# Optimization experiments

Measured on AMD Instinct MI355X. Metric: run time of the kernel, lower is better.

## Reference

```python
import jax, jax.numpy as jnp
import numpy as np

NUM_HEADS = 4
NUM_GROUPS = 8
EPS = 1e-5


def group_norm(x, w, b):
    # x: (B, C, H, W); normalize per group of C//NUM_GROUPS channels
    B, C, H, W = x.shape
    xg = x.reshape(B, NUM_GROUPS, C // NUM_GROUPS, H, W)
    mean = xg.mean(axis=(2, 3, 4), keepdims=True)
    var = xg.var(axis=(2, 3, 4), keepdims=True)
    xn = ((xg - mean) * jax.lax.rsqrt(var + EPS)).reshape(B, C, H, W)
    return xn * w[None, :, None, None] + b[None, :, None, None]


def conv1x1(x, w, b):
    # x: (B, C_in, H, W), w: (C_out, C_in), b: (C_out,)
    return jnp.einsum('bchw,oc->bohw', x, w) + b[None, :, None, None]


def setup_inputs() -> dict:
    key = jax.random.key(0)
    B, C, H, W = 4, 256, 64, 64
    k1, k2, k3 = jax.random.split(key, 3)
    scale = 1.0 / np.sqrt(C)
    return {
        'x': jax.random.normal(k1, (B, C, H, W), dtype=jnp.float32),
        'norm_w': jnp.ones((C,), dtype=jnp.float32),
        'norm_b': jnp.zeros((C,), dtype=jnp.float32),
        'qkv_w': jax.random.normal(k2, (3 * C, C), dtype=jnp.float32) * scale,
        'qkv_b': jnp.zeros((3 * C,), dtype=jnp.float32),
        'proj_w': jax.random.normal(k3, (C, C), dtype=jnp.float32) * scale,
        'proj_b': jnp.zeros((C,), dtype=jnp.float32),
    }


def reference(x, norm_w, norm_b, qkv_w, qkv_b, proj_w, proj_b):
    B, C, H, W = x.shape
    hd = C // NUM_HEADS  # head dim
    h = group_norm(x, norm_w, norm_b)
    qkv = conv1x1(h, qkv_w, qkv_b)            # (B, 3C, H, W)
    q, k, v = jnp.split(qkv, 3, axis=1)
    q = q.reshape(B, NUM_HEADS, hd, H * W)
    k = k.reshape(B, NUM_HEADS, hd, H * W)
    v = v.reshape(B, NUM_HEADS, hd, H * W)
    attn = jnp.einsum('bhcn,bhcm->bhnm', q, k) / jnp.sqrt(jnp.asarray(hd, x.dtype))
    attn = jax.nn.softmax(attn, axis=-1)
    out = jnp.einsum('bhnm,bhcm->bhcn', attn, v).reshape(B, C, H, W)
    out = conv1x1(out, proj_w, proj_b)
    return x + out
```

## Files before the change

### kernel.cpp

```cpp
#include <hip/hip_runtime.h>
#include <hip/hip_bf16.h>
#include <stdint.h>


#define B_  4
#define C_  256
#define N_  4096
#define NH_ 4
#define HD_ 64
#define G_  8
#define CPG_ 32
#define GRP_ELEMS (CPG_ * N_)

typedef __attribute__((ext_vector_type(8))) short short8;
typedef __attribute__((ext_vector_type(4))) float f32x4;
typedef __attribute__((ext_vector_type(4))) unsigned short us4;

__device__ __forceinline__ unsigned short f2bf(float f) {
  union { float f; unsigned u; } v; v.f = f;
  unsigned r = v.u + 0x7FFFu + ((v.u >> 16) & 1u);
  return (unsigned short)(r >> 16);
}

__device__ __forceinline__ unsigned pkbf2(float a, float b) {
  __hip_bfloat162 h = __float22bfloat162_rn(make_float2(a, b));
  unsigned r; __builtin_memcpy(&r, &h, sizeof(r)); return r;
}

__device__ __forceinline__ void dma16(const unsigned short* g, unsigned short* l) {
  __builtin_amdgcn_global_load_lds(
      (const __attribute__((address_space(1))) unsigned int*)(g),
      (__attribute__((address_space(3))) unsigned int*)(l), 16, 0, 0);
}

__global__ void cvt_weights(const float* __restrict__ qkvw,
                            const float* __restrict__ projw,
                            unsigned short* __restrict__ wq,
                            unsigned short* __restrict__ wp) {
  int i = blockIdx.x * 256 + threadIdx.x;
  if (i < 768 * 256) wq[i] = f2bf(qkvw[i]);
  if (i < 256 * 256) wp[i] = f2bf(projw[i]);
}

__global__ void gn_partial(const float* __restrict__ x, float* __restrict__ partial) {
  int idx = blockIdx.x;
  int slice = idx & 15, g = (idx >> 4) & 7, b = idx >> 7;
  int t = threadIdx.x;
  const float* base = x + (size_t)(b * C_ + g * CPG_) * N_ + slice * 256;
  float s = 0.f, sq = 0.f;
#pragma unroll
  for (int cc = 0; cc < CPG_; cc++) {
    float v = base[(size_t)cc * N_ + t];
    s += v; sq += v * v;
  }
#pragma unroll
  for (int off = 32; off; off >>= 1) {
    s  += __shfl_down(s,  off, 64);
    sq += __shfl_down(sq, off, 64);
  }
  __shared__ float ls[8];
  int wave = t >> 6, lane = t & 63;
  if (lane == 0) { ls[wave * 2] = s; ls[wave * 2 + 1] = sq; }
  __syncthreads();
  if (t == 0) {
    float S = ls[0] + ls[2] + ls[4] + ls[6];
    float SQ = ls[1] + ls[3] + ls[5] + ls[7];
    partial[idx * 2] = S; partial[idx * 2 + 1] = SQ;
  }
}

__global__ void gn_finalize(const float* __restrict__ partial, float* __restrict__ stats) {
  int t = threadIdx.x;
  if (t < 32) {
    float s = 0.f, sq = 0.f;
    for (int i = 0; i < 16; i++) {
      s  += partial[(t * 16 + i) * 2];
      sq += partial[(t * 16 + i) * 2 + 1];
    }
    const float inv = 1.0f / (float)GRP_ELEMS;
    float mean = s * inv;
    float var = sq * inv - mean * mean;
    stats[t * 2] = mean;
    stats[t * 2 + 1] = rsqrtf(var + 1e-5f);
  }
}

__global__ void gn_apply(const float* __restrict__ x,
                         const float* __restrict__ nw, const float* __restrict__ nb,
                         const float* __restrict__ stats, unsigned short* __restrict__ hT) {
  int nt = blockIdx.x, ct = blockIdx.y, b = blockIdx.z;
  __shared__ unsigned short tile[32][72];
  int t = threadIdx.x;
  int n_loc = t & 63, c_loc = t >> 6;
  float mean = stats[(b * G_ + ct) * 2];
  float rstd = stats[(b * G_ + ct) * 2 + 1];
  const float* xb = x + (size_t)(b * C_ + ct * CPG_) * N_ + nt * 64;
#pragma unroll
  for (int rr = 0; rr < 8; rr++) {
    int cc = rr * 4 + c_loc;
    int c = ct * CPG_ + cc;
    float v = xb[(size_t)cc * N_ + n_loc];
    v = (v - mean) * rstd * nw[c] + nb[c];
    tile[cc][n_loc] = f2bf(v);
  }
  __syncthreads();
  int c2 = t & 31, n2 = t >> 5;
  unsigned short* out = hT + ((size_t)(b * N_ + nt * 64)) * C_ + ct * CPG_ + c2;
#pragma unroll
  for (int pass = 0; pass < 8; pass++) {
    int n = pass * 8 + n2;
    out[(size_t)n * C_] = tile[c2][n];
  }
}

__global__ __launch_bounds__(256) void qkv_gemm(
    const unsigned short* __restrict__ hT, const unsigned short* __restrict__ wq,
    const float* __restrict__ qb,
    unsigned short* __restrict__ Qt, unsigned short* __restrict__ Kt,
    unsigned short* __restrict__ V) {
  int nt = blockIdx.x, ot = blockIdx.y, b = blockIdx.z;
  int t = threadIdx.x;
  int wave = t >> 6, lane = t & 63, l15 = lane & 15, quad = lane >> 4, l7 = l15 & 7;
  int o_base = ot * 64 + wave * 16;

  __shared__ __align__(16) unsigned short sh[64 * C_];

  {
    int row0 = wave * 2 + (lane >> 5);
    int col8 = lane & 31;
    int src8 = (col8 & 24) | ((col8 & 7) ^ (row0 & 7));
    const unsigned short* gsrc = hT + ((size_t)(b * N_ + nt * 64 + row0)) * C_ + src8 * 8;
#pragma unroll
    for (int it = 0; it < 8; it++)
      dma16(gsrc + (size_t)it * 8 * C_, sh + (it * 8 + wave * 2) * C_);
  }

  f32x4 acc[4];
#pragma unroll
  for (int tt = 0; tt < 4; tt++) acc[tt] = (f32x4){0.f, 0.f, 0.f, 0.f};

  const short8* arow = reinterpret_cast<const short8*>(wq + (size_t)(o_base + l15) * C_);

  asm volatile("s_waitcnt vmcnt(0)" ::: "memory");
  __syncthreads();

#pragma unroll
  for (int kk = 0; kk < 8; kk++) {
    short8 a = arow[kk * 4 + quad];
    int g = kk * 4 + quad;
    int col8 = (g & 24) | ((g & 7) ^ l7);
#pragma unroll
    for (int tt = 0; tt < 4; tt++) {
      short8 bf = *reinterpret_cast<const short8*>(&sh[(tt * 16 + l15) * C_ + col8 * 8]);
      acc[tt] = __builtin_amdgcn_mfma_f32_16x16x32_bf16(a, bf, acc[tt], 0, 0, 0);
    }
  }

  int sec = ot >> 2, head = ot & 3;
  int cw = wave * 16 + quad * 4;
  int bh = b * NH_ + head;
  const float SC = 0.125f * 1.44269504088896340736f;

  if (sec == 0) {
#pragma unroll
    for (int tt = 0; tt < 4; tt++) {
      int n = nt * 64 + tt * 16 + l15;
      us4 pk;
#pragma unroll
      for (int i = 0; i < 4; i++)
        pk[i] = f2bf((acc[tt][i] + qb[ot * 64 + cw + i]) * SC);
      *reinterpret_cast<us4*>(Qt + ((size_t)bh * N_ + n) * HD_ + cw) = pk;
    }
  } else if (sec == 1) {
#pragma unroll
    for (int tt = 0; tt < 4; tt++) {
      int n = nt * 64 + tt * 16 + l15;
      us4 pk;
#pragma unroll
      for (int i = 0; i < 4; i++)
        pk[i] = f2bf(acc[tt][i] + qb[ot * 64 + cw + i]);
      *reinterpret_cast<us4*>(Kt + ((size_t)bh * N_ + n) * HD_ + cw) = pk;
    }
  } else {
#pragma unroll
    for (int tt = 0; tt < 4; tt++) {
      int n = nt * 64 + tt * 16 + l15;
#pragma unroll
      for (int i = 0; i < 4; i++)
        V[((size_t)bh * HD_ + cw + i) * N_ + n] = f2bf(acc[tt][i] + qb[ot * 64 + cw + i]);
    }
  }
}

__global__ __launch_bounds__(256, 2) void flash_attn(
    const unsigned short* __restrict__ Qt, const unsigned short* __restrict__ Kt,
    const unsigned short* __restrict__ Vv, unsigned short* __restrict__ aoT) {
  int bh = blockIdx.x & 15, qt = blockIdx.x >> 4;
  int b = bh >> 2, head = bh & 3;
  int t = threadIdx.x;
  int wave = t >> 6, lane = t & 63, l15 = lane & 15, quad = lane >> 4;
  int l7 = l15 & 7;
  int qsub = wave >> 1, khalf = wave & 1;

  const unsigned short* Qb = Qt + (size_t)bh * N_ * HD_;
  const unsigned short* Kb = Kt + (size_t)bh * N_ * HD_;
  const unsigned short* Vb = Vv + (size_t)bh * HD_ * N_;
  int q_base = qt * 128 + qsub * 64;

  __shared__ __align__(16) unsigned char smem[74752];
  unsigned short* Ks = (unsigned short*)smem;
  unsigned short* Vs = (unsigned short*)(smem + 32768);
  unsigned short* Ps = (unsigned short*)(smem + 65536);
  float* Obuf = (float*)smem;
  float* lbuf = (float*)(smem + 34816);

  const short8 vones = {(short)0x3F80, (short)0x3F80, (short)0x3F80, (short)0x3F80,
                        (short)0x3F80, (short)0x3F80, (short)0x3F80, (short)0x3F80};

  short8 qf[4][2];
#pragma unroll
  for (int r = 0; r < 4; r++)
#pragma unroll
    for (int h = 0; h < 2; h++)
      qf[r][h] = *reinterpret_cast<const short8*>(
          Qb + (size_t)(q_base + r * 16 + l15) * HD_ + h * 32 + quad * 8);

  f32x4 oa[4][4], la[4];
#pragma unroll
  for (int r = 0; r < 4; r++) {
    la[r] = (f32x4){0.f, 0.f, 0.f, 0.f};
#pragma unroll
    for (int ct = 0; ct < 4; ct++) oa[r][ct] = (f32x4){0.f, 0.f, 0.f, 0.f};
  }

  int i8 = lane >> 3, e = lane & 7;
  int perm = (e ^ i8) * 8;
  int kvoff = (khalf * 2) * 4096;
  auto stage = [&](int kt2, int buf) {
    int m0 = khalf * 2048 + kt2 * 64;
    unsigned short* Kd = Ks + kvoff + buf * 4096;
    unsigned short* Vd = Vs + kvoff + buf * 4096;
#pragma unroll
    for (int cc = 0; cc < 4; cc++) {
      int c = qsub * 4 + cc;
      dma16(Kb + (size_t)(m0 + c * 8 + i8) * HD_ + perm, Kd + c * 512);
      dma16(Vb + (size_t)(c * 8 + i8) * N_ + m0 + perm, Vd + c * 512);
    }
  };

  stage(0, 0);

  unsigned short* Pw = Ps + wave * 16 * 72;

#pragma unroll 1
  for (int kt = 0; kt < 32; kt++) {
    int buf = kt & 1;
    asm volatile("s_waitcnt vmcnt(0)" ::: "memory");
    __builtin_amdgcn_s_barrier();
    if (kt + 1 < 32) stage(kt + 1, buf ^ 1);

    const unsigned short* Kbuf = Ks + kvoff + buf * 4096;
    const unsigned short* Vbuf = Vs + kvoff + buf * 4096;

    short8 kf[4][2], vf[4][2];
#pragma unroll
    for (int tt = 0; tt < 4; tt++)
#pragma unroll
      for (int kh2 = 0; kh2 < 2; kh2++) {
        kf[tt][kh2] = *reinterpret_cast<const short8*>(
            &Kbuf[(tt * 16 + l15) * 64 + (((kh2 * 4 + quad) ^ l7) * 8)]);
        vf[tt][kh2] = *reinterpret_cast<const short8*>(
            &Vbuf[(tt * 16 + l15) * 64 + (((kh2 * 4 + quad) ^ l7) * 8)]);
      }

#pragma unroll
    for (int r = 0; r < 4; r++) {
      f32x4 s[4];
#pragma unroll
      for (int tt = 0; tt < 4; tt++) {
        f32x4 z = (f32x4){0.f, 0.f, 0.f, 0.f};
        z = __builtin_amdgcn_mfma_f32_16x16x32_bf16(kf[tt][0], qf[r][0], z, 0, 0, 0);
        s[tt] = __builtin_amdgcn_mfma_f32_16x16x32_bf16(kf[tt][1], qf[r][1], z, 0, 0, 0);
      }
#pragma unroll
      for (int tt = 0; tt < 4; tt++) {
        union { unsigned u2[2]; us4 v; } w;
        w.u2[0] = pkbf2(__builtin_amdgcn_exp2f(s[tt][0]), __builtin_amdgcn_exp2f(s[tt][1]));
        w.u2[1] = pkbf2(__builtin_amdgcn_exp2f(s[tt][2]), __builtin_amdgcn_exp2f(s[tt][3]));
        *reinterpret_cast<us4*>(&Pw[l15 * 72 + tt * 16 + quad * 4]) = w.v;
      }
      short8 pf0 = *reinterpret_cast<const short8*>(&Pw[l15 * 72 + quad * 8]);
      short8 pf1 = *reinterpret_cast<const short8*>(&Pw[l15 * 72 + 32 + quad * 8]);
#pragma unroll
      for (int ct = 0; ct < 4; ct++) {
        oa[r][ct] = __builtin_amdgcn_mfma_f32_16x16x32_bf16(vf[ct][0], pf0, oa[r][ct], 0, 0, 0);
        oa[r][ct] = __builtin_amdgcn_mfma_f32_16x16x32_bf16(vf[ct][1], pf1, oa[r][ct], 0, 0, 0);
      }
      la[r] = __builtin_amdgcn_mfma_f32_16x16x32_bf16(vones, pf0, la[r], 0, 0, 0);
      la[r] = __builtin_amdgcn_mfma_f32_16x16x32_bf16(vones, pf1, la[r], 0, 0, 0);
    }
  }

  __builtin_amdgcn_s_barrier();
  if (khalf == 1) {
#pragma unroll
    for (int r = 0; r < 4; r++) {
#pragma unroll
      for (int ct = 0; ct < 4; ct++)
#pragma unroll
        for (int i = 0; i < 4; i++)
          Obuf[qsub * 4352 + (ct * 16 + quad * 4 + i) * 68 + r * 16 + l15] = oa[r][ct][i];
      if (quad == 0) lbuf[qsub * 64 + r * 16 + l15] = la[r][0];
    }
  }
  __builtin_amdgcn_s_barrier();
  if (khalf == 0) {
#pragma unroll
    for (int r = 0; r < 4; r++) {
      float inv = 1.0f / (la[r][0] + lbuf[qsub * 64 + r * 16 + l15]);
      int n = q_base + r * 16 + l15;
#pragma unroll
      for (int ct = 0; ct < 4; ct++) {
        const float* ob = &Obuf[qsub * 4352 + (ct * 16 + quad * 4) * 68 + r * 16 + l15];
        union { unsigned u2[2]; us4 v; } w;
        w.u2[0] = pkbf2((oa[r][ct][0] + ob[0]) * inv, (oa[r][ct][1] + ob[68]) * inv);
        w.u2[1] = pkbf2((oa[r][ct][2] + ob[136]) * inv, (oa[r][ct][3] + ob[204]) * inv);
        *reinterpret_cast<us4*>(
            aoT + ((size_t)(b * N_ + n)) * C_ + head * HD_ + ct * 16 + quad * 4) = w.v;
      }
    }
  }
}

__global__ __launch_bounds__(256) void proj_gemm(
    const unsigned short* __restrict__ aoT, const unsigned short* __restrict__ wp,
    const float* __restrict__ pb, const float* __restrict__ x,
    float* __restrict__ out) {
  int nt = blockIdx.x, ot = blockIdx.y, b = blockIdx.z;
  int t = threadIdx.x;
  int wave = t >> 6, lane = t & 63, l15 = lane & 15, quad = lane >> 4, l7 = l15 & 7;
  int o_base = ot * 64 + wave * 16;

  __shared__ __align__(16) unsigned short sh[64 * C_];

  {
    int row0 = wave * 2 + (lane >> 5);
    int col8 = lane & 31;
    int src8 = (col8 & 24) | ((col8 & 7) ^ (row0 & 7));
    const unsigned short* gsrc = aoT + ((size_t)(b * N_ + nt * 64 + row0)) * C_ + src8 * 8;
#pragma unroll
    for (int it = 0; it < 8; it++)
      dma16(gsrc + (size_t)it * 8 * C_, sh + (it * 8 + wave * 2) * C_);
  }

  f32x4 acc[4];
#pragma unroll
  for (int tt = 0; tt < 4; tt++) acc[tt] = (f32x4){0.f, 0.f, 0.f, 0.f};

  const short8* arow = reinterpret_cast<const short8*>(wp + (size_t)(o_base + l15) * C_);

  asm volatile("s_waitcnt vmcnt(0)" ::: "memory");
  __syncthreads();

#pragma unroll
  for (int kk = 0; kk < 8; kk++) {
    short8 a = arow[kk * 4 + quad];
    int g = kk * 4 + quad;
    int col8 = (g & 24) | ((g & 7) ^ l7);
#pragma unroll
    for (int tt = 0; tt < 4; tt++) {
      short8 bf = *reinterpret_cast<const short8*>(&sh[(tt * 16 + l15) * C_ + col8 * 8]);
      acc[tt] = __builtin_amdgcn_mfma_f32_16x16x32_bf16(a, bf, acc[tt], 0, 0, 0);
    }
  }
#pragma unroll
  for (int tt = 0; tt < 4; tt++) {
    int n = nt * 64 + tt * 16 + l15;
#pragma unroll
    for (int i = 0; i < 4; i++) {
      int o = o_base + quad * 4 + i;
      size_t idx = ((size_t)(b * C_ + o)) * N_ + n;
      out[idx] = acc[tt][i] + pb[o] + x[idx];
    }
  }
}

extern "C" void kernel_launch(void* const* d_in, const int* in_sizes, int n_in,
                              void* d_out, int out_size, void* d_ws, size_t ws_size,
                              hipStream_t stream) {
  const float* x      = (const float*)d_in[0];
  const float* norm_w = (const float*)d_in[1];
  const float* norm_b = (const float*)d_in[2];
  const float* qkv_w  = (const float*)d_in[3];
  const float* qkv_b  = (const float*)d_in[4];
  const float* proj_w = (const float*)d_in[5];
  const float* proj_b = (const float*)d_in[6];
  float* out = (float*)d_out;

  char* ws = (char*)d_ws;
  size_t off = 0;
  auto alloc = [&](size_t bytes) { size_t o = off; off = (off + bytes + 255) & ~(size_t)255; return o; };
  size_t off_partial = alloc(512 * 2 * sizeof(float));
  size_t off_stats   = alloc(32 * 2 * sizeof(float));
  size_t off_wq      = alloc((size_t)768 * 256 * 2);
  size_t off_wp      = alloc((size_t)256 * 256 * 2);
  size_t off_hT      = alloc((size_t)B_ * N_ * C_ * 2);
  size_t off_Qt      = alloc((size_t)B_ * NH_ * N_ * HD_ * 2);
  size_t off_Kt      = alloc((size_t)B_ * NH_ * N_ * HD_ * 2);
  size_t off_V       = alloc((size_t)B_ * NH_ * HD_ * N_ * 2);
  size_t off_aoT     = alloc((size_t)B_ * N_ * C_ * 2);

  float* partial = (float*)(ws + off_partial);
  float* stats   = (float*)(ws + off_stats);
  unsigned short* wq  = (unsigned short*)(ws + off_wq);
  unsigned short* wp  = (unsigned short*)(ws + off_wp);
  unsigned short* hT  = (unsigned short*)(ws + off_hT);
  unsigned short* Qt  = (unsigned short*)(ws + off_Qt);
  unsigned short* Kt  = (unsigned short*)(ws + off_Kt);
  unsigned short* V   = (unsigned short*)(ws + off_V);
  unsigned short* aoT = (unsigned short*)(ws + off_aoT);

  cvt_weights<<<768, 256, 0, stream>>>(qkv_w, proj_w, wq, wp);
  gn_partial<<<512, 256, 0, stream>>>(x, partial);
  gn_finalize<<<1, 64, 0, stream>>>(partial, stats);
  gn_apply<<<dim3(64, 8, 4), 256, 0, stream>>>(x, norm_w, norm_b, stats, hT);
  qkv_gemm<<<dim3(64, 12, 4), 256, 0, stream>>>(hT, wq, qkv_b, Qt, Kt, V);
  flash_attn<<<512, 256, 0, stream>>>(Qt, Kt, V, aoT);
  proj_gemm<<<dim3(64, 4, 4), 256, 0, stream>>>(aoT, wp, proj_b, x, out);
}
```

Before: 200.8 us.

## Retile QKV/proj GEMMs for more outputs per block and split flash-attn keys across four waves

The QKV GEMM now has each block compute a whole 256-channel section (one head per wave), and the projection GEMM computes 128 output channels per block. Both reuse each staged activation fragment across several weight rows and launch fewer blocks. Flash attention drops to 64 queries per block, with each of the four waves handling a quarter of the keys from its own private K/V buffer, no per-iteration block barrier, and a tree reduction of partial outputs at the end. It also uses less shared memory, allowing three blocks per CU, at the cost of a larger reduction and less-hidden single-buffer loads.

```diff
diff --git a/kernel.cpp b/kernel.cpp
--- a/kernel.cpp
+++ b/kernel.cpp
@@ -118,13 +118,11 @@
     const float* __restrict__ qb,
     unsigned short* __restrict__ Qt, unsigned short* __restrict__ Kt,
     unsigned short* __restrict__ V) {
-  int nt = blockIdx.x, ot = blockIdx.y, b = blockIdx.z;
+  int nt = blockIdx.x, sec = blockIdx.y, b = blockIdx.z;
   int t = threadIdx.x;
   int wave = t >> 6, lane = t & 63, l15 = lane & 15, quad = lane >> 4, l7 = l15 & 7;
-  int o_base = ot * 64 + wave * 16;
 
   __shared__ __align__(16) unsigned short sh[64 * C_];
-
   {
     int row0 = wave * 2 + (lane >> 5);
     int col8 = lane & 31;
@@ -135,64 +133,87 @@
       dma16(gsrc + (size_t)it * 8 * C_, sh + (it * 8 + wave * 2) * C_);
   }
 
-  f32x4 acc[4];
-#pragma unroll
-  for (int tt = 0; tt < 4; tt++) acc[tt] = (f32x4){0.f, 0.f, 0.f, 0.f};
-
-  const short8* arow = reinterpret_cast<const short8*>(wq + (size_t)(o_base + l15) * C_);
+  f32x4 acc[4][4];
+#pragma unroll
+  for (int r = 0; r < 4; r++)
+#pragma unroll
+    for (int tt = 0; tt < 4; tt++) acc[r][tt] = (f32x4){0.f, 0.f, 0.f, 0.f};
+
+  const short8* arow[4];
+#pragma unroll
+  for (int r = 0; r < 4; r++)
+    arow[r] = reinterpret_cast<const short8*>(
+        wq + (size_t)(sec * 256 + wave * 64 + r * 16 + l15) * C_);
 
   asm volatile("s_waitcnt vmcnt(0)" ::: "memory");
   __syncthreads();
 
 #pragma unroll
   for (int kk = 0; kk < 8; kk++) {
-    short8 a = arow[kk * 4 + quad];
     int g = kk * 4 + quad;
     int col8 = (g & 24) | ((g & 7) ^ l7);
-#pragma unroll
-    for (int tt = 0; tt < 4; tt++) {
-      short8 bf = *reinterpret_cast<const short8*>(&sh[(tt * 16 + l15) * C_ + col8 * 8]);
-      acc[tt] = __builtin_amdgcn_mfma_f32_16x16x32_bf16(a, bf, acc[tt], 0, 0, 0);
-    }
-  }
-
-  int sec = ot >> 2, head = ot & 3;
-  int cw = wave * 16 + quad * 4;
+    short8 bfr[4];
+#pragma unroll
+    for (int tt = 0; tt < 4; tt++)
+      bfr[tt] = *reinterpret_cast<const short8*>(&sh[(tt * 16 + l15) * C_ + col8 * 8]);
+#pragma unroll
+    for (int r = 0; r < 4; r++) {
+      short8 a = arow[r][g];
+#pragma unroll
+      for (int tt = 0; tt < 4; tt++)
+        acc[r][tt] = __builtin_amdgcn_mfma_f32_16x16x32_bf16(a, bfr[tt], acc[r][tt], 0, 0, 0);
+    }
+  }
+
+  int head = wave;
   int bh = b * NH_ + head;
   const float SC = 0.125f * 1.44269504088896340736f;
 
   if (sec == 0) {
 #pragma unroll
-    for (int tt = 0; tt < 4; tt++) {
-      int n = nt * 64 + tt * 16 + l15;
-      us4 pk;
-#pragma unroll
-      for (int i = 0; i < 4; i++)
-        pk[i] = f2bf((acc[tt][i] + qb[ot * 64 + cw + i]) * SC);
-      *reinterpret_cast<us4*>(Qt + ((size_t)bh * N_ + n) * HD_ + cw) = pk;
+    for (int r = 0; r < 4; r++) {
+      int cw = r * 16 + quad * 4;
+#pragma unroll
+      for (int tt = 0; tt < 4; tt++) {
+        int n = nt * 64 + tt * 16 + l15;
+        us4 pk;
+#pragma unroll
+        for (int i = 0; i < 4; i++)
+          pk[i] = f2bf((acc[r][tt][i] + qb[wave * 64 + cw + i]) * SC);
+        *reinterpret_cast<us4*>(Qt + ((size_t)bh * N_ + n) * HD_ + cw) = pk;
+      }
     }
   } else if (sec == 1) {
 #pragma unroll
-    for (int tt = 0; tt < 4; tt++) {
-      int n = nt * 64 + tt * 16 + l15;
-      us4 pk;
-#pragma unroll
-      for (int i = 0; i < 4; i++)
-        pk[i] = f2bf(acc[tt][i] + qb[ot * 64 + cw + i]);
-      *reinterpret_cast<us4*>(Kt + ((size_t)bh * N_ + n) * HD_ + cw) = pk;
+    for (int r = 0; r < 4; r++) {
+      int cw = r * 16 + quad * 4;
+#pragma unroll
+      for (int tt = 0; tt < 4; tt++) {
+        int n = nt * 64 + tt * 16 + l15;
+        us4 pk;
+#pragma unroll
+        for (int i = 0; i < 4; i++)
+          pk[i] = f2bf(acc[r][tt][i] + qb[256 + wave * 64 + cw + i]);
+        *reinterpret_cast<us4*>(Kt + ((size_t)bh * N_ + n) * HD_ + cw) = pk;
+      }
     }
   } else {
 #pragma unroll
-    for (int tt = 0; tt < 4; tt++) {
-      int n = nt * 64 + tt * 16 + l15;
-#pragma unroll
-      for (int i = 0; i < 4; i++)
-        V[((size_t)bh * HD_ + cw + i) * N_ + n] = f2bf(acc[tt][i] + qb[ot * 64 + cw + i]);
-    }
-  }
-}
-
-__global__ __launch_bounds__(256, 2) void flash_attn(
+    for (int r = 0; r < 4; r++) {
+      int cw = r * 16 + quad * 4;
+#pragma unroll
+      for (int tt = 0; tt < 4; tt++) {
+        int n = nt * 64 + tt * 16 + l15;
+#pragma unroll
+        for (int i = 0; i < 4; i++)
+          V[((size_t)bh * HD_ + cw + i) * N_ + n] =
+              f2bf(acc[r][tt][i] + qb[512 + wave * 64 + cw + i]);
+      }
+    }
+  }
+}
+
+__global__ __launch_bounds__(256, 3) void flash_attn(
     const unsigned short* __restrict__ Qt, const unsigned short* __restrict__ Kt,
     const unsigned short* __restrict__ Vv, unsigned short* __restrict__ aoT) {
   int bh = blockIdx.x & 15, qt = blockIdx.x >> 4;
@@ -200,19 +221,20 @@
   int t = threadIdx.x;
   int wave = t >> 6, lane = t & 63, l15 = lane & 15, quad = lane >> 4;
   int l7 = l15 & 7;
-  int qsub = wave >> 1, khalf = wave & 1;
 
   const unsigned short* Qb = Qt + (size_t)bh * N_ * HD_;
   const unsigned short* Kb = Kt + (size_t)bh * N_ * HD_;
   const unsigned short* Vb = Vv + (size_t)bh * HD_ * N_;
-  int q_base = qt * 128 + qsub * 64;
-
-  __shared__ __align__(16) unsigned char smem[74752];
-  unsigned short* Ks = (unsigned short*)smem;
-  unsigned short* Vs = (unsigned short*)(smem + 32768);
-  unsigned short* Ps = (unsigned short*)(smem + 65536);
-  float* Obuf = (float*)smem;
-  float* lbuf = (float*)(smem + 34816);
+  int q_base = qt * 64;
+
+  __shared__ __align__(16) unsigned char smem[39936];
+  unsigned short* Kw = (unsigned short*)(smem + wave * 4096);
+  unsigned short* Vw = (unsigned short*)(smem + 16384 + wave * 4096);
+  unsigned short* Pw = (unsigned short*)(smem + 32768 + wave * 1792);
+  float* ObA = (float*)smem;
+  float* ObB = (float*)(smem + 17408);
+  float* lbA = (float*)(smem + 34816);
+  float* lbB = (float*)(smem + 35072);
 
   const short8 vones = {(short)0x3F80, (short)0x3F80, (short)0x3F80, (short)0x3F80,
                         (short)0x3F80, (short)0x3F80, (short)0x3F80, (short)0x3F80};
@@ -233,95 +255,121 @@
     for (int ct = 0; ct < 4; ct++) oa[r][ct] = (f32x4){0.f, 0.f, 0.f, 0.f};
   }
 
-  int i8 = lane >> 3, e = lane & 7;
-  int perm = (e ^ i8) * 8;
-  int kvoff = (khalf * 2) * 4096;
-  auto stage = [&](int kt2, int buf) {
-    int m0 = khalf * 2048 + kt2 * 64;
-    unsigned short* Kd = Ks + kvoff + buf * 4096;
-    unsigned short* Vd = Vs + kvoff + buf * 4096;
-#pragma unroll
-    for (int cc = 0; cc < 4; cc++) {
-      int c = qsub * 4 + cc;
-      dma16(Kb + (size_t)(m0 + c * 8 + i8) * HD_ + perm, Kd + c * 512);
-      dma16(Vb + (size_t)(c * 8 + i8) * N_ + m0 + perm, Vd + c * 512);
-    }
+  int key0 = wave * 1024;
+  int i8 = lane >> 3, e8 = lane & 7;
+  int r16 = lane >> 2, e4 = lane & 3;
+  int kperm = (e8 ^ i8) * 8;
+  int vperm = (e4 ^ ((r16 >> 1) & 3)) * 8;
+
+  auto stage = [&](int kt2) {
+    int m0 = key0 + kt2 * 32;
+#pragma unroll
+    for (int cc = 0; cc < 4; cc++)
+      dma16(Kb + (size_t)(m0 + cc * 8 + i8) * HD_ + kperm, Kw + cc * 512);
+#pragma unroll
+    for (int cc = 0; cc < 4; cc++)
+      dma16(Vb + (size_t)(cc * 16 + r16) * N_ + m0 + vperm, Vw + cc * 512);
   };
 
-  stage(0, 0);
-
-  unsigned short* Pw = Ps + wave * 16 * 72;
+  stage(0);
 
 #pragma unroll 1
   for (int kt = 0; kt < 32; kt++) {
-    int buf = kt & 1;
     asm volatile("s_waitcnt vmcnt(0)" ::: "memory");
-    __builtin_amdgcn_s_barrier();
-    if (kt + 1 < 32) stage(kt + 1, buf ^ 1);
-
-    const unsigned short* Kbuf = Ks + kvoff + buf * 4096;
-    const unsigned short* Vbuf = Vs + kvoff + buf * 4096;
-
-    short8 kf[4][2], vf[4][2];
-#pragma unroll
-    for (int tt = 0; tt < 4; tt++)
-#pragma unroll
-      for (int kh2 = 0; kh2 < 2; kh2++) {
-        kf[tt][kh2] = *reinterpret_cast<const short8*>(
-            &Kbuf[(tt * 16 + l15) * 64 + (((kh2 * 4 + quad) ^ l7) * 8)]);
-        vf[tt][kh2] = *reinterpret_cast<const short8*>(
-            &Vbuf[(tt * 16 + l15) * 64 + (((kh2 * 4 + quad) ^ l7) * 8)]);
-      }
-
-#pragma unroll
-    for (int r = 0; r < 4; r++) {
-      f32x4 s[4];
-#pragma unroll
-      for (int tt = 0; tt < 4; tt++) {
+
+    short8 kf[2][2];
+#pragma unroll
+    for (int tt = 0; tt < 2; tt++)
+#pragma unroll
+      for (int kh = 0; kh < 2; kh++)
+        kf[tt][kh] = *reinterpret_cast<const short8*>(
+            &Kw[(tt * 16 + l15) * 64 + (((kh * 4 + quad) ^ l7) * 8)]);
+    short8 vf[4];
+#pragma unroll
+    for (int ct = 0; ct < 4; ct++)
+      vf[ct] = *reinterpret_cast<const short8*>(
+          &Vw[(ct * 16 + l15) * 32 + ((quad ^ ((l15 >> 1) & 3)) * 8)]);
+
+    asm volatile("s_waitcnt lgkmcnt(0)" ::: "memory");
+    if (kt + 1 < 32) stage(kt + 1);
+
+#pragma unroll
+    for (int r = 0; r < 4; r++) {
+      f32x4 s0, s1;
+      {
         f32x4 z = (f32x4){0.f, 0.f, 0.f, 0.f};
-        z = __builtin_amdgcn_mfma_f32_16x16x32_bf16(kf[tt][0], qf[r][0], z, 0, 0, 0);
-        s[tt] = __builtin_amdgcn_mfma_f32_16x16x32_bf16(kf[tt][1], qf[r][1], z, 0, 0, 0);
-      }
-#pragma unroll
-      for (int tt = 0; tt < 4; tt++) {
-        union { unsigned u2[2]; us4 v; } w;
-        w.u2[0] = pkbf2(__builtin_amdgcn_exp2f(s[tt][0]), __builtin_amdgcn_exp2f(s[tt][1]));
-        w.u2[1] = pkbf2(__builtin_amdgcn_exp2f(s[tt][2]), __builtin_amdgcn_exp2f(s[tt][3]));
-        *reinterpret_cast<us4*>(&Pw[l15 * 72 + tt * 16 + quad * 4]) = w.v;
-      }
-      short8 pf0 = *reinterpret_cast<const short8*>(&Pw[l15 * 72 + quad * 8]);
-      short8 pf1 = *reinterpret_cast<const short8*>(&Pw[l15 * 72 + 32 + quad * 8]);
+        z  = __builtin_amdgcn_mfma_f32_16x16x32_bf16(kf[0][0], qf[r][0], z, 0, 0, 0);
+        s0 = __builtin_amdgcn_mfma_f32_16x16x32_bf16(kf[0][1], qf[r][1], z, 0, 0, 0);
+      }
+      {
+        f32x4 z = (f32x4){0.f, 0.f, 0.f, 0.f};
+        z  = __builtin_amdgcn_mfma_f32_16x16x32_bf16(kf[1][0], qf[r][0], z, 0, 0, 0);
+        s1 = __builtin_amdgcn_mfma_f32_16x16x32_bf16(kf[1][1], qf[r][1], z, 0, 0, 0);
+      }
+      union { unsigned u2[2]; us4 v; } w0, w1;
+      w0.u2[0] = pkbf2(__builtin_amdgcn_exp2f(s0[0]), __builtin_amdgcn_exp2f(s0[1]));
+      w0.u2[1] = pkbf2(__builtin_amdgcn_exp2f(s0[2]), __builtin_amdgcn_exp2f(s0[3]));
+      w1.u2[0] = pkbf2(__builtin_amdgcn_exp2f(s1[0]), __builtin_amdgcn_exp2f(s1[1]));
+      w1.u2[1] = pkbf2(__builtin_amdgcn_exp2f(s1[2]), __builtin_amdgcn_exp2f(s1[3]));
+      *reinterpret_cast<us4*>(&Pw[l15 * 56 + quad * 4]) = w0.v;
+      *reinterpret_cast<us4*>(&Pw[l15 * 56 + 16 + quad * 4]) = w1.v;
+      short8 pf = *reinterpret_cast<const short8*>(&Pw[l15 * 56 + quad * 8]);
+#pragma unroll
+      for (int ct = 0; ct < 4; ct++)
+        oa[r][ct] = __builtin_amdgcn_mfma_f32_16x16x32_bf16(vf[ct], pf, oa[r][ct], 0, 0, 0);
+      la[r] = __builtin_amdgcn_mfma_f32_16x16x32_bf16(vones, pf, la[r], 0, 0, 0);
+    }
+  }
+
+  __syncthreads();
+  if (wave == 1 || wave == 3) {
+    float* Ob = (wave == 1) ? ObA : ObB;
+    float* lb = (wave == 1) ? lbA : lbB;
+#pragma unroll
+    for (int r = 0; r < 4; r++) {
+#pragma unroll
+      for (int ct = 0; ct < 4; ct++)
+#pragma unroll
+        for (int i = 0; i < 4; i++)
+          Ob[(ct * 16 + quad * 4 + i) * 68 + r * 16 + l15] = oa[r][ct][i];
+      if (quad == 0) lb[r * 16 + l15] = la[r][0];
+    }
+  }
+  __syncthreads();
+  if (wave == 0 || wave == 2) {
+    const float* Ob = (wave == 0) ? ObA : ObB;
+    const float* lb = (wave == 0) ? lbA : lbB;
+#pragma unroll
+    for (int r = 0; r < 4; r++) {
+      la[r][0] += lb[r * 16 + l15];
+#pragma unroll
+      for (int ct = 0; ct < 4; ct++)
+#pragma unroll
+        for (int i = 0; i < 4; i++)
+          oa[r][ct][i] += Ob[(ct * 16 + quad * 4 + i) * 68 + r * 16 + l15];
+    }
+  }
+  __syncthreads();
+  if (wave == 2) {
+#pragma unroll
+    for (int r = 0; r < 4; r++) {
+#pragma unroll
+      for (int ct = 0; ct < 4; ct++)
+#pragma unroll
+        for (int i = 0; i < 4; i++)
+          ObA[(ct * 16 + quad * 4 + i) * 68 + r * 16 + l15] = oa[r][ct][i];
+      if (quad == 0) lbA[r * 16 + l15] = la[r][0];
+    }
+  }
+  __syncthreads();
+  if (wave == 0) {
+#pragma unroll
+    for (int r = 0; r < 4; r++) {
+      float inv = 1.0f / (la[r][0] + lbA[r * 16 + l15]);
+      int n = q_base + r * 16 + l15;
 #pragma unroll
       for (int ct = 0; ct < 4; ct++) {
-        oa[r][ct] = __builtin_amdgcn_mfma_f32_16x16x32_bf16(vf[ct][0], pf0, oa[r][ct], 0, 0, 0);
-        oa[r][ct] = __builtin_amdgcn_mfma_f32_16x16x32_bf16(vf[ct][1], pf1, oa[r][ct], 0, 0, 0);
-      }
-      la[r] = __builtin_amdgcn_mfma_f32_16x16x32_bf16(vones, pf0, la[r], 0, 0, 0);
-      la[r] = __builtin_amdgcn_mfma_f32_16x16x32_bf16(vones, pf1, la[r], 0, 0, 0);
-    }
-  }
-
-  __builtin_amdgcn_s_barrier();
-  if (khalf == 1) {
-#pragma unroll
-    for (int r = 0; r < 4; r++) {
-#pragma unroll
-      for (int ct = 0; ct < 4; ct++)
-#pragma unroll
-        for (int i = 0; i < 4; i++)
-          Obuf[qsub * 4352 + (ct * 16 + quad * 4 + i) * 68 + r * 16 + l15] = oa[r][ct][i];
-      if (quad == 0) lbuf[qsub * 64 + r * 16 + l15] = la[r][0];
-    }
-  }
-  __builtin_amdgcn_s_barrier();
-  if (khalf == 0) {
-#pragma unroll
-    for (int r = 0; r < 4; r++) {
-      float inv = 1.0f / (la[r][0] + lbuf[qsub * 64 + r * 16 + l15]);
-      int n = q_base + r * 16 + l15;
-#pragma unroll
-      for (int ct = 0; ct < 4; ct++) {
-        const float* ob = &Obuf[qsub * 4352 + (ct * 16 + quad * 4) * 68 + r * 16 + l15];
+        const float* ob = &ObA[(ct * 16 + quad * 4) * 68 + r * 16 + l15];
         union { unsigned u2[2]; us4 v; } w;
         w.u2[0] = pkbf2((oa[r][ct][0] + ob[0]) * inv, (oa[r][ct][1] + ob[68]) * inv);
         w.u2[1] = pkbf2((oa[r][ct][2] + ob[136]) * inv, (oa[r][ct][3] + ob[204]) * inv);
@@ -339,10 +387,9 @@
   int nt = blockIdx.x, ot = blockIdx.y, b = blockIdx.z;
   int t = threadIdx.x;
   int wave = t >> 6, lane = t & 63, l15 = lane & 15, quad = lane >> 4, l7 = l15 & 7;
-  int o_base = ot * 64 + wave * 16;
+  int o_base = ot * 128 + wave * 32;
 
   __shared__ __align__(16) unsigned short sh[64 * C_];
-
   {
     int row0 = wave * 2 + (lane >> 5);
     int col8 = lane & 31;
@@ -353,36 +400,48 @@
       dma16(gsrc + (size_t)it * 8 * C_, sh + (it * 8 + wave * 2) * C_);
   }
 
-  f32x4 acc[4];
-#pragma unroll
-  for (int tt = 0; tt < 4; tt++) acc[tt] = (f32x4){0.f, 0.f, 0.f, 0.f};
-
-  const short8* arow = reinterpret_cast<const short8*>(wp + (size_t)(o_base + l15) * C_);
+  f32x4 acc[2][4];
+#pragma unroll
+  for (int r = 0; r < 2; r++)
+#pragma unroll
+    for (int tt = 0; tt < 4; tt++) acc[r][tt] = (f32x4){0.f, 0.f, 0.f, 0.f};
+
+  const short8* arow[2];
+#pragma unroll
+  for (int r = 0; r < 2; r++)
+    arow[r] = reinterpret_cast<const short8*>(wp + (size_t)(o_base + r * 16 + l15) * C_);
 
   asm volatile("s_waitcnt vmcnt(0)" ::: "memory");
   __syncthreads();
 
 #pragma unroll
   for (int kk = 0; kk < 8; kk++) {
-    short8 a = arow[kk * 4 + quad];
     int g = kk * 4 + quad;
     int col8 = (g & 24) | ((g & 7) ^ l7);
+    short8 bfr[4];
+#pragma unroll
+    for (int tt = 0; tt < 4; tt++)
+      bfr[tt] = *reinterpret_cast<const short8*>(&sh[(tt * 16 + l15) * C_ + col8 * 8]);
+#pragma unroll
+    for (int r = 0; r < 2; r++) {
+      short8 a = arow[r][g];
+#pragma unroll
+      for (int tt = 0; tt < 4; tt++)
+        acc[r][tt] = __builtin_amdgcn_mfma_f32_16x16x32_bf16(a, bfr[tt], acc[r][tt], 0, 0, 0);
+    }
+  }
+#pragma unroll
+  for (int r = 0; r < 2; r++)
 #pragma unroll
     for (int tt = 0; tt < 4; tt++) {
-      short8 bf = *reinterpret_cast<const short8*>(&sh[(tt * 16 + l15) * C_ + col8 * 8]);
-      acc[tt] = __builtin_amdgcn_mfma_f32_16x16x32_bf16(a, bf, acc[tt], 0, 0, 0);
-    }
-  }
-#pragma unroll
-  for (int tt = 0; tt < 4; tt++) {
-    int n = nt * 64 + tt * 16 + l15;
-#pragma unroll
-    for (int i = 0; i < 4; i++) {
-      int o = o_base + quad * 4 + i;
-      size_t idx = ((size_t)(b * C_ + o)) * N_ + n;
-      out[idx] = acc[tt][i] + pb[o] + x[idx];
-    }
-  }
+      int n = nt * 64 + tt * 16 + l15;
+#pragma unroll
+      for (int i = 0; i < 4; i++) {
+        int o = o_base + r * 16 + quad * 4 + i;
+        size_t idx = ((size_t)(b * C_ + o)) * N_ + n;
+        out[idx] = acc[r][tt][i] + pb[o] + x[idx];
+      }
+    }
 }
 
 extern "C" void kernel_launch(void* const* d_in, const int* in_sizes, int n_in,
@@ -424,7 +483,7 @@
   gn_partial<<<512, 256, 0, stream>>>(x, partial);
   gn_finalize<<<1, 64, 0, stream>>>(partial, stats);
   gn_apply<<<dim3(64, 8, 4), 256, 0, stream>>>(x, norm_w, norm_b, stats, hT);
-  qkv_gemm<<<dim3(64, 12, 4), 256, 0, stream>>>(hT, wq, qkv_b, Qt, Kt, V);
-  flash_attn<<<512, 256, 0, stream>>>(Qt, Kt, V, aoT);
-  proj_gemm<<<dim3(64, 4, 4), 256, 0, stream>>>(aoT, wp, proj_b, x, out);
-}
+  qkv_gemm<<<dim3(64, 3, 4), 256, 0, stream>>>(hT, wq, qkv_b, Qt, Kt, V);
+  flash_attn<<<1024, 256, 0, stream>>>(Qt, Kt, V, aoT);
+  proj_gemm<<<dim3(64, 2, 4), 256, 0, stream>>>(aoT, wp, proj_b, x, out);
+}
```

Measured after the change: 223.1 us. 1.11x slower.
